# Kernel optimization log

Hardware: AMD Instinct MI355X
Metric: run time of the kernel (lower is better)

The kernel has to match this reference:

```python
import jax, jax.numpy as jnp
import numpy as np

BN_EPS = 1e-3      # Keras BatchNormalization default epsilon
LRELU_ALPHA = 0.3  # Keras LeakyReLU default alpha


def _bn(x, gamma, beta, mean, var):
    # inference-mode batch norm over the feature (last) axis
    return gamma * (x - mean) * jax.lax.rsqrt(var + BN_EPS) + beta


def _gcn(x, adj, w, b):
    # spektral GCNConv: A_hat @ (X @ W) + b   (adj assumed pre-normalized)
    xw = jnp.einsum('bnf,fc->bnc', x, w)
    return jnp.einsum('bnm,bmc->bnc', adj, xw) + b


def _lrelu(x):
    return jnp.where(x >= 0, x, LRELU_ALPHA * x)


def setup_inputs() -> dict:
    key = jax.random.key(0)
    ks = jax.random.split(key, 12)
    B, N, C = 16, 1024, 256
    x = jax.random.normal(ks[0], (B, N, C), dtype=jnp.float32)
    # roughly row-normalized dense adjacency (stands in for D^-1/2 (A+I) D^-1/2)
    adj = jax.random.uniform(ks[1], (B, N, N), dtype=jnp.float32) / N
    s = 1.0 / np.sqrt(C)
    return {
        'x': x,
        'adj': adj,
        'bn1_gamma': jnp.ones((C,), jnp.float32),
        'bn1_beta': jnp.zeros((C,), jnp.float32),
        'bn1_mean': jax.random.normal(ks[2], (C,), jnp.float32) * 0.1,
        'bn1_var': jax.random.uniform(ks[3], (C,), jnp.float32) + 0.5,
        'w1': jax.random.normal(ks[4], (C, C), jnp.float32) * s,
        'b1': jnp.zeros((C,), jnp.float32),
        'bn2_gamma': jnp.ones((C,), jnp.float32),
        'bn2_beta': jnp.zeros((C,), jnp.float32),
        'bn2_mean': jax.random.normal(ks[5], (C,), jnp.float32) * 0.1,
        'bn2_var': jax.random.uniform(ks[6], (C,), jnp.float32) + 0.5,
        'w2': jax.random.normal(ks[7], (C, C), jnp.float32) * s,
        'b2': jnp.zeros((C,), jnp.float32),
        'w_skip': jax.random.normal(ks[8], (C, C), jnp.float32) * s,
        'b_skip': jnp.zeros((C,), jnp.float32),
    }


def reference(x, adj, bn1_gamma, bn1_beta, bn1_mean, bn1_var, w1, b1,
              bn2_gamma, bn2_beta, bn2_mean, bn2_var, w2, b2, w_skip, b_skip):
    h = _bn(x, bn1_gamma, bn1_beta, bn1_mean, bn1_var)          # BN(input)
    out = _lrelu(_gcn(h, adj, w1, b1))                          # GCNConv + LeakyReLU
    out = _bn(out, bn2_gamma, bn2_beta, bn2_mean, bn2_var)      # BN
    out = _lrelu(_gcn(out, adj, w2, b2))                        # GCNConv + LeakyReLU
    skip = _gcn(h, adj, w_skip, b_skip)                         # skip GCNConv on BN(input)
    # Dropout is identity at inference
    return out + skip
```

## Files before the change

### kernel.cpp

```cpp
#include <hip/hip_runtime.h>

#define LRELU_ALPHA 0.3f
#define BN_EPS 1e-3f

using u16 = unsigned short;
using u32 = unsigned int;

typedef __attribute__((ext_vector_type(8))) short bf16x8;
typedef __attribute__((ext_vector_type(4))) float f32x4;

struct alignas(8) U16x4 { u16 x, y, z, w; };

__device__ __forceinline__ u16 f2bf(float f) {
  union { float f; u32 u; } v; v.f = f;
  u32 b = v.u;
  b += 0x7FFFu + ((b >> 16) & 1u);
  return (u16)(b >> 16);
}
__device__ __forceinline__ float bf2f(u16 h) {
  union { u32 u; float f; } v; v.u = ((u32)h) << 16;
  return v.f;
}

typedef const __attribute__((address_space(1))) void* gas_ptr;
typedef __attribute__((address_space(3))) void* las_ptr;

__device__ __forceinline__ void gload16(const void* g, void* l) {
  __builtin_amdgcn_global_load_lds((gas_ptr)g, (las_ptr)l, 16, 0, 0);
}

__device__ __forceinline__ int xcd_swz512(int lid) {
  return (lid & 7) * 64 + (lid >> 3);
}

template <int K>
__device__ __forceinline__ void gemm_core(const u16* __restrict__ A,
                                          const u16* __restrict__ B,
                                          u16* lds, f32x4 (&acc)[4][4]) {
  const int t = threadIdx.x, lane = t & 63, wid = t >> 6;
  const int wm = (wid >> 1) * 64, wn = (wid & 1) * 64;
  const int lrow = lane & 15, lk = (lane >> 4) * 8;
  const int r0 = t >> 3, ce = (t & 7) * 8, lo = wid * 512;
  u16* ldsA = lds;
  u16* ldsB = lds + 8192;
#pragma unroll 1
  for (int kt = 0; kt < K / 64; ++kt) {
    const u16* gA = A + kt * 64;
    const u16* gB = B + kt * 64;
#pragma unroll
    for (int cc = 0; cc < 4; ++cc) {
      gload16(gA + (size_t)(cc * 32 + r0) * K + ce, ldsA + cc * 2048 + lo);
      gload16(gB + (size_t)(cc * 32 + r0) * K + ce, ldsB + cc * 2048 + lo);
    }
    asm volatile("s_waitcnt vmcnt(0)" ::: "memory");
    __syncthreads();
#pragma unroll
    for (int kk = 0; kk < 2; ++kk) {
      bf16x8 a[4], b[4];
#pragma unroll
      for (int i = 0; i < 4; ++i)
        a[i] = *(const bf16x8*)(ldsA + (wm + i * 16 + lrow) * 64 + kk * 32 + lk);
#pragma unroll
      for (int i = 0; i < 4; ++i)
        b[i] = *(const bf16x8*)(ldsB + (wn + i * 16 + lrow) * 64 + kk * 32 + lk);
#pragma unroll
      for (int i = 0; i < 4; ++i)
#pragma unroll
        for (int j = 0; j < 4; ++j)
          acc[i][j] = __builtin_amdgcn_mfma_f32_16x16x32_bf16(a[i], b[j], acc[i][j], 0, 0, 0);
    }
    __syncthreads();
  }
}

template <int K>
__device__ __forceinline__ void gemm_core64(const u16* __restrict__ A,
                                            const u16* __restrict__ B,
                                            u16* lds, f32x4 (&acc)[2][4]) {
  const int t = threadIdx.x, lane = t & 63, wid = t >> 6;
  const int wm = wid * 32;
  const int lrow = lane & 15, lk = (lane >> 4) * 8;
  const int r0 = t >> 3, ce = (t & 7) * 8, lo = wid * 512;
  u16* ldsA = lds;
  u16* ldsB = lds + 8192;
#pragma unroll 1
  for (int kt = 0; kt < K / 64; ++kt) {
    const u16* gA = A + kt * 64;
    const u16* gB = B + kt * 64;
#pragma unroll
    for (int cc = 0; cc < 4; ++cc)
      gload16(gA + (size_t)(cc * 32 + r0) * K + ce, ldsA + cc * 2048 + lo);
#pragma unroll
    for (int cc = 0; cc < 2; ++cc)
      gload16(gB + (size_t)(cc * 32 + r0) * K + ce, ldsB + cc * 2048 + lo);
    asm volatile("s_waitcnt vmcnt(0)" ::: "memory");
    __syncthreads();
#pragma unroll
    for (int kk = 0; kk < 2; ++kk) {
      bf16x8 a[2], b[4];
#pragma unroll
      for (int i = 0; i < 2; ++i)
        a[i] = *(const bf16x8*)(ldsA + (wm + i * 16 + lrow) * 64 + kk * 32 + lk);
#pragma unroll
      for (int j = 0; j < 4; ++j)
        b[j] = *(const bf16x8*)(ldsB + (j * 16 + lrow) * 64 + kk * 32 + lk);
#pragma unroll
      for (int i = 0; i < 2; ++i)
#pragma unroll
        for (int j = 0; j < 4; ++j)
          acc[i][j] = __builtin_amdgcn_mfma_f32_16x16x32_bf16(a[i], b[j], acc[i][j], 0, 0, 0);
    }
    __syncthreads();
  }
}

template <int K>
__device__ __forceinline__ void gemm_core64x2(const u16* __restrict__ A,
                                              const u16* __restrict__ B1,
                                              const u16* __restrict__ B2,
                                              u16* lds, f32x4 (&acc1)[2][4],
                                              f32x4 (&acc2)[2][4]) {
  const int t = threadIdx.x, lane = t & 63, wid = t >> 6;
  const int wm = wid * 32;
  const int lrow = lane & 15, lk = (lane >> 4) * 8;
  const int r0 = t >> 3, ce = (t & 7) * 8, lo = wid * 512;
  u16* ldsA  = lds;
  u16* ldsB1 = lds + 8192;
  u16* ldsB2 = lds + 12288;
#pragma unroll 1
  for (int kt = 0; kt < K / 64; ++kt) {
    const u16* gA  = A  + kt * 64;
    const u16* gB1 = B1 + kt * 64;
    const u16* gB2 = B2 + kt * 64;
#pragma unroll
    for (int cc = 0; cc < 4; ++cc)
      gload16(gA + (size_t)(cc * 32 + r0) * K + ce, ldsA + cc * 2048 + lo);
#pragma unroll
    for (int cc = 0; cc < 2; ++cc) {
      gload16(gB1 + (size_t)(cc * 32 + r0) * K + ce, ldsB1 + cc * 2048 + lo);
      gload16(gB2 + (size_t)(cc * 32 + r0) * K + ce, ldsB2 + cc * 2048 + lo);
    }
    asm volatile("s_waitcnt vmcnt(0)" ::: "memory");
    __syncthreads();
#pragma unroll
    for (int kk = 0; kk < 2; ++kk) {
      bf16x8 a[2], b1[4], b2[4];
#pragma unroll
      for (int i = 0; i < 2; ++i)
        a[i] = *(const bf16x8*)(ldsA + (wm + i * 16 + lrow) * 64 + kk * 32 + lk);
#pragma unroll
      for (int j = 0; j < 4; ++j) {
        b1[j] = *(const bf16x8*)(ldsB1 + (j * 16 + lrow) * 64 + kk * 32 + lk);
        b2[j] = *(const bf16x8*)(ldsB2 + (j * 16 + lrow) * 64 + kk * 32 + lk);
      }
#pragma unroll
      for (int i = 0; i < 2; ++i)
#pragma unroll
        for (int j = 0; j < 4; ++j) {
          acc1[i][j] = __builtin_amdgcn_mfma_f32_16x16x32_bf16(a[i], b1[j], acc1[i][j], 0, 0, 0);
          acc2[i][j] = __builtin_amdgcn_mfma_f32_16x16x32_bf16(a[i], b2[j], acc2[i][j], 0, 0, 0);
        }
    }
    __syncthreads();
  }
}

#define ACC_INIT_N(name, R)                          \
  f32x4 name[R][4];                                  \
  _Pragma("unroll") for (int i_ = 0; i_ < R; ++i_)   \
  _Pragma("unroll") for (int j_ = 0; j_ < 4; ++j_)   \
      name[i_][j_] = {0.f, 0.f, 0.f, 0.f};

__global__ __launch_bounds__(256) void k_pre(
    const float* __restrict__ w1, const float* __restrict__ wsk, const float* __restrict__ w2,
    const float* __restrict__ g1, const float* __restrict__ be1,
    const float* __restrict__ m1, const float* __restrict__ v1,
    const float* __restrict__ g2, const float* __restrict__ be2,
    const float* __restrict__ m2, const float* __restrict__ v2,
    const float* __restrict__ x, const float* __restrict__ adj,
    u16* __restrict__ wcatT, u16* __restrict__ w2T,
    float* __restrict__ s2, float* __restrict__ t2c,
    u16* __restrict__ h_bf, u16* __restrict__ adj_bf) {
  int bid = blockIdx.x;
  if (bid < 768) {
    if (bid == 0) {
      int c = threadIdx.x;
      float a2 = g2[c] * rsqrtf(v2[c] + BN_EPS);
      s2[c] = a2;
      t2c[c] = be2[c] - m2[c] * a2;
    }
    int i = bid * 256 + threadIdx.x;
    if (i < 131072) {
      int co = i >> 8, ci = i & 255;
      const float* w = (co < 256) ? w1 : wsk;
      wcatT[i] = f2bf(w[ci * 256 + (co & 255)]);
    } else {
      int k = i - 131072;
      int co = k >> 8, ci = k & 255;
      w2T[k] = f2bf(w2[ci * 256 + co]);
    }
  } else if (bid < 1024) {
    int base = (bid - 768) * 256 + threadIdx.x;
    int c0 = (base << 2) & 255;
    float sc[4], sh[4];
#pragma unroll
    for (int u = 0; u < 4; ++u) {
      int c = c0 + u;
      float a = g1[c] * rsqrtf(v1[c] + BN_EPS);
      sc[u] = a;
      sh[u] = be1[c] - m1[c] * a;
    }
#pragma unroll
    for (int j = 0; j < 16; ++j) {
      int k = j * 65536 + base;
      float4 v = ((const float4*)x)[k];
      U16x4 o = {f2bf(v.x * sc[0] + sh[0]), f2bf(v.y * sc[1] + sh[1]),
                 f2bf(v.z * sc[2] + sh[2]), f2bf(v.w * sc[3] + sh[3])};
      ((U16x4*)h_bf)[k] = o;
    }
  } else {
    const int N4 = 4194304;
    int idx = (bid - 1024) * 256 + threadIdx.x;
    const int stride = 2048 * 256;
#pragma unroll 1
    for (; idx < N4; idx += stride) {
      float4 v = ((const float4*)adj)[idx];
      U16x4 o = {f2bf(v.x), f2bf(v.y), f2bf(v.z), f2bf(v.w)};
      ((U16x4*)adj_bf)[idx] = o;
    }
  }
}

__global__ __launch_bounds__(256) void k_xw(const u16* __restrict__ h_bf,
                                            const u16* __restrict__ wcatT,
                                            u16* __restrict__ hwT) {
  __shared__ u16 lds[17408];
  const int wg = xcd_swz512(blockIdx.x);
  const int mt = wg >> 2, nt = wg & 3;
  ACC_INIT_N(acc, 4);
  gemm_core<256>(h_bf + (size_t)mt * 128 * 256, wcatT + (size_t)nt * 128 * 256, lds, acc);

  const int t = threadIdx.x, lane = t & 63, wid = t >> 6;
  const int row0 = (wid >> 1) * 64 + (lane >> 4) * 4;
  const int col0 = (wid & 1) * 64 + (lane & 15);
  __syncthreads();
  u16* tl = lds;
#pragma unroll
  for (int j = 0; j < 4; ++j) {
    int co_l = col0 + j * 16;
#pragma unroll
    for (int i = 0; i < 4; ++i)
#pragma unroll
      for (int q = 0; q < 4; ++q)
        tl[co_l * 136 + row0 + i * 16 + q] = f2bf(acc[i][j][q]);
  }
  __syncthreads();
  const int rw = t >> 4, seg = t & 15;
  const int b = mt >> 3, nb = (mt & 7) * 128;
#pragma unroll
  for (int p = 0; p < 8; ++p) {
    int co_l = p * 16 + rw;
    *(bf16x8*)(hwT + (((size_t)(b * 512 + nt * 128 + co_l)) << 10) + nb + seg * 8) =
        *(const bf16x8*)(tl + co_l * 136 + seg * 8);
  }
}

__global__ __launch_bounds__(256) void k_big1(const u16* __restrict__ adj_bf,
                                              const u16* __restrict__ hwT,
                                              const float* __restrict__ b1,
                                              const float* __restrict__ s2,
                                              const float* __restrict__ t2c,
                                              u16* __restrict__ u2b) {
  __shared__ u16 lds[17408];
  ACC_INIT_N(acc, 2);
  const int wg = xcd_swz512(blockIdx.x);
  const int mt = wg & 7, nt = (wg >> 3) & 3, bz = wg >> 5;
  gemm_core64<1024>(adj_bf + ((size_t)bz << 20) + (size_t)mt * 128 * 1024,
                    hwT    + ((size_t)bz << 19) + ((size_t)(nt * 64) << 10), lds, acc);

  const int t = threadIdx.x, lane = t & 63, wid = t >> 6;
  const int row0 = wid * 32 + (lane >> 4) * 4;
  const int col0 = lane & 15;
  __syncthreads();
  u16* tl = lds;
#pragma unroll
  for (int j = 0; j < 4; ++j) {
    int cl = col0 + j * 16;
    int c = nt * 64 + cl;
    float bias = b1[c], sc = s2[c], tc = t2c[c];
#pragma unroll
    for (int i = 0; i < 2; ++i)
#pragma unroll
      for (int q = 0; q < 4; ++q) {
        float y = acc[i][j][q] + bias;
        float u = (y >= 0.f) ? y : LRELU_ALPHA * y;
        tl[(row0 + i * 16 + q) * 72 + cl] = f2bf(fmaf(u, sc, tc));
      }
  }
  __syncthreads();
  u16* dstbase = u2b + ((size_t)bz << 18) + nt * 64;
  const int rw = t >> 3, seg = t & 7;
#pragma unroll
  for (int p = 0; p < 4; ++p) {
    int nl = p * 32 + rw;
    *(bf16x8*)(dstbase + ((size_t)(mt * 128 + nl) << 8) + seg * 8) =
        *(const bf16x8*)(tl + nl * 72 + seg * 8);
  }
}

__global__ __launch_bounds__(256) void k_sm2(const u16* __restrict__ w2T,
                                             const u16* __restrict__ u2b,
                                             u16* __restrict__ t2T) {
  __shared__ u16 lds[12288];
  ACC_INIT_N(acc, 2);
  const int mt = blockIdx.x, nt = blockIdx.y, bz = blockIdx.z;
  gemm_core64<256>(w2T + (size_t)mt * 128 * 256,
                   u2b + ((size_t)bz << 18) + (size_t)nt * 64 * 256, lds, acc);

  const int t = threadIdx.x, lane = t & 63, wid = t >> 6;
  const int row0 = wid * 32 + (lane >> 4) * 4;
  const int col0 = lane & 15;
  __syncthreads();
  u16* tl = lds;
#pragma unroll
  for (int j = 0; j < 4; ++j)
#pragma unroll
    for (int i = 0; i < 2; ++i)
#pragma unroll
      for (int q = 0; q < 4; ++q)
        tl[(row0 + i * 16 + q) * 72 + col0 + j * 16] = f2bf(acc[i][j][q]);
  __syncthreads();
  u16* base = t2T + ((size_t)bz << 18) + nt * 64;
  const int rw = t >> 3, seg = t & 7;
#pragma unroll
  for (int p = 0; p < 4; ++p) {
    int co = p * 32 + rw;
    *(bf16x8*)(base + (((size_t)(mt * 128 + co)) << 10) + seg * 8) =
        *(const bf16x8*)(tl + co * 72 + seg * 8);
  }
}

__global__ __launch_bounds__(256) void k_big2(const u16* __restrict__ adj_bf,
                                              const u16* __restrict__ t2T,
                                              const u16* __restrict__ hwT,
                                              const float* __restrict__ b2,
                                              const float* __restrict__ bsk,
                                              float* __restrict__ outp) {
  __shared__ u16 lds[17408];
  ACC_INIT_N(acc1, 2);
  ACC_INIT_N(acc2, 2);
  const int wg = xcd_swz512(blockIdx.x);
  const int mt = wg & 7, nt = (wg >> 3) & 3, bz = wg >> 5;
  gemm_core64x2<1024>(adj_bf + ((size_t)bz << 20) + (size_t)mt * 128 * 1024,
                      t2T    + ((size_t)bz << 18) + ((size_t)(nt * 64) << 10),
                      hwT    + ((size_t)bz << 19) + ((size_t)(256 + nt * 64) << 10),
                      lds, acc1, acc2);

  const int t = threadIdx.x, lane = t & 63, wid = t >> 6;
  const int row0 = wid * 32 + (lane >> 4) * 4;
  const int col0 = lane & 15;
  __syncthreads();
  float* tf = (float*)lds;
#pragma unroll
  for (int j = 0; j < 4; ++j) {
    int cl = col0 + j * 16;
    int c = nt * 64 + cl;
    float bc = b2[c], bs = bsk[c];
#pragma unroll
    for (int i = 0; i < 2; ++i)
#pragma unroll
      for (int q = 0; q < 4; ++q) {
        float y = acc1[i][j][q] + bc;
        float conv = (y >= 0.f) ? y : LRELU_ALPHA * y;
        tf[(row0 + i * 16 + q) * 68 + cl] = conv + acc2[i][j][q] + bs;
      }
  }
  __syncthreads();
  const int rw = t >> 4, seg = t & 15;
#pragma unroll
  for (int p = 0; p < 8; ++p) {
    int nl = p * 16 + rw;
    size_t go = ((size_t)bz << 18) + ((size_t)(mt * 128 + nl) << 8) + nt * 64 + seg * 4;
    *(float4*)(outp + go) = *(const float4*)(tf + nl * 68 + seg * 4);
  }
}

extern "C" void kernel_launch(void* const* d_in, const int* in_sizes, int n_in,
                              void* d_out, int out_size, void* d_ws, size_t ws_size,
                              hipStream_t stream) {
  const float* x   = (const float*)d_in[0];
  const float* adj = (const float*)d_in[1];
  const float* g1  = (const float*)d_in[2];
  const float* be1 = (const float*)d_in[3];
  const float* mu1 = (const float*)d_in[4];
  const float* v1  = (const float*)d_in[5];
  const float* w1  = (const float*)d_in[6];
  const float* b1  = (const float*)d_in[7];
  const float* g2  = (const float*)d_in[8];
  const float* be2 = (const float*)d_in[9];
  const float* mu2 = (const float*)d_in[10];
  const float* v2  = (const float*)d_in[11];
  const float* w2  = (const float*)d_in[12];
  const float* b2  = (const float*)d_in[13];
  const float* wsk = (const float*)d_in[14];
  const float* bsk = (const float*)d_in[15];
  float* out = (float*)d_out;

  char* ws = (char*)d_ws;
  u16*   adj_bf = (u16*)(ws);
  u16*   hwT    = (u16*)(ws + 33554432);
  u16*   h_bf   = (u16*)(ws + 50331648);
  u16*   u2b    = (u16*)(ws + 58720256);
  u16*   t2T    = (u16*)(ws + 67108864);
  u16*   wcatT  = (u16*)(ws + 83886080);
  u16*   w2T    = (u16*)(ws + 84148224);
  float* s2     = (float*)(ws + 84281344);
  float* t2c    = (float*)(ws + 84282368);
  if (ws_size < 84283392) return;

  k_pre  <<<3072, 256, 0, stream>>>(w1, wsk, w2, g1, be1, mu1, v1, g2, be2, mu2, v2,
                                    x, adj, wcatT, w2T, s2, t2c, h_bf, adj_bf);
  k_xw   <<<512,  256, 0, stream>>>(h_bf, wcatT, hwT);
  k_big1 <<<512,  256, 0, stream>>>(adj_bf, hwT, b1, s2, t2c, u2b);
  k_sm2  <<<dim3(2, 16, 16), 256, 0, stream>>>(w2T, u2b, t2T);
  k_big2 <<<512,  256, 0, stream>>>(adj_bf, t2T, hwT, b2, bsk, out);
}
```

Before: 205.4 us.

## Fuse all stages into one persistent kernel with global atomic barriers

Merges the five kernels (convert/BN prep, X@W, first adjacency GEMM, W2 GEMM, second adjacency GEMM) into a single persistent 512-block kernel separated by software grid barriers built on atomics in workspace. The X@W stage is re-tiled to 64-wide output tiles, with each block doing two tiles. The goal is to remove kernel launch gaps and tail effects between stages. In exchange it adds a memset, global spin barriers and threadfences, and relies on all 512 blocks being co-resident; the prep stage also runs with fewer blocks than before.

```diff
diff --git a/kernel.cpp b/kernel.cpp
--- a/kernel.cpp
+++ b/kernel.cpp
@@ -17,10 +17,6 @@
   b += 0x7FFFu + ((b >> 16) & 1u);
   return (u16)(b >> 16);
 }
-__device__ __forceinline__ float bf2f(u16 h) {
-  union { u32 u; float f; } v; v.u = ((u32)h) << 16;
-  return v.f;
-}
 
 typedef const __attribute__((address_space(1))) void* gas_ptr;
 typedef __attribute__((address_space(3))) void* las_ptr;
@@ -33,44 +29,15 @@
   return (lid & 7) * 64 + (lid >> 3);
 }
 
-template <int K>
-__device__ __forceinline__ void gemm_core(const u16* __restrict__ A,
-                                          const u16* __restrict__ B,
-                                          u16* lds, f32x4 (&acc)[4][4]) {
-  const int t = threadIdx.x, lane = t & 63, wid = t >> 6;
-  const int wm = (wid >> 1) * 64, wn = (wid & 1) * 64;
-  const int lrow = lane & 15, lk = (lane >> 4) * 8;
-  const int r0 = t >> 3, ce = (t & 7) * 8, lo = wid * 512;
-  u16* ldsA = lds;
-  u16* ldsB = lds + 8192;
-#pragma unroll 1
-  for (int kt = 0; kt < K / 64; ++kt) {
-    const u16* gA = A + kt * 64;
-    const u16* gB = B + kt * 64;
-#pragma unroll
-    for (int cc = 0; cc < 4; ++cc) {
-      gload16(gA + (size_t)(cc * 32 + r0) * K + ce, ldsA + cc * 2048 + lo);
-      gload16(gB + (size_t)(cc * 32 + r0) * K + ce, ldsB + cc * 2048 + lo);
-    }
-    asm volatile("s_waitcnt vmcnt(0)" ::: "memory");
-    __syncthreads();
-#pragma unroll
-    for (int kk = 0; kk < 2; ++kk) {
-      bf16x8 a[4], b[4];
-#pragma unroll
-      for (int i = 0; i < 4; ++i)
-        a[i] = *(const bf16x8*)(ldsA + (wm + i * 16 + lrow) * 64 + kk * 32 + lk);
-#pragma unroll
-      for (int i = 0; i < 4; ++i)
-        b[i] = *(const bf16x8*)(ldsB + (wn + i * 16 + lrow) * 64 + kk * 32 + lk);
-#pragma unroll
-      for (int i = 0; i < 4; ++i)
-#pragma unroll
-        for (int j = 0; j < 4; ++j)
-          acc[i][j] = __builtin_amdgcn_mfma_f32_16x16x32_bf16(a[i], b[j], acc[i][j], 0, 0, 0);
-    }
-    __syncthreads();
-  }
+__device__ __forceinline__ void gbar(u32* bar, u32 nwg) {
+  __threadfence();
+  __syncthreads();
+  if (threadIdx.x == 0) {
+    atomicAdd(bar, 1u);
+    while (atomicAdd(bar, 0u) < nwg) __builtin_amdgcn_s_sleep(2);
+  }
+  __syncthreads();
+  __threadfence();
 }
 
 template <int K>
@@ -171,217 +138,205 @@
   _Pragma("unroll") for (int j_ = 0; j_ < 4; ++j_)   \
       name[i_][j_] = {0.f, 0.f, 0.f, 0.f};
 
-__global__ __launch_bounds__(256) void k_pre(
+__global__ __launch_bounds__(256, 2) void k_fused(
     const float* __restrict__ w1, const float* __restrict__ wsk, const float* __restrict__ w2,
     const float* __restrict__ g1, const float* __restrict__ be1,
     const float* __restrict__ m1, const float* __restrict__ v1,
     const float* __restrict__ g2, const float* __restrict__ be2,
     const float* __restrict__ m2, const float* __restrict__ v2,
     const float* __restrict__ x, const float* __restrict__ adj,
+    const float* __restrict__ b1, const float* __restrict__ b2,
+    const float* __restrict__ bsk,
     u16* __restrict__ wcatT, u16* __restrict__ w2T,
     float* __restrict__ s2, float* __restrict__ t2c,
-    u16* __restrict__ h_bf, u16* __restrict__ adj_bf) {
-  int bid = blockIdx.x;
-  if (bid < 768) {
-    if (bid == 0) {
-      int c = threadIdx.x;
+    u16* __restrict__ h_bf, u16* __restrict__ adj_bf,
+    u16* __restrict__ hwT, u16* __restrict__ u2b, u16* __restrict__ t2T,
+    u32* __restrict__ bars,
+    float* __restrict__ outp) {
+  __shared__ u16 lds[17408];
+  const int bidx = blockIdx.x;
+  const int t = threadIdx.x;
+  const int lane = t & 63, wid = t >> 6;
+
+  {
+    const int N4 = 4194304;
+#pragma unroll 1
+    for (int idx = bidx * 256 + t; idx < N4; idx += 131072) {
+      float4 v = ((const float4*)adj)[idx];
+      U16x4 o = {f2bf(v.x), f2bf(v.y), f2bf(v.z), f2bf(v.w)};
+      ((U16x4*)adj_bf)[idx] = o;
+    }
+    {
+      int idx0 = bidx * 256 + t;
+      int c0 = (idx0 << 2) & 255;
+      float sc[4], sh[4];
+#pragma unroll
+      for (int u = 0; u < 4; ++u) {
+        int c = c0 + u;
+        float a = g1[c] * rsqrtf(v1[c] + BN_EPS);
+        sc[u] = a;
+        sh[u] = be1[c] - m1[c] * a;
+      }
+#pragma unroll 1
+      for (int idx = idx0; idx < 1048576; idx += 131072) {
+        float4 v = ((const float4*)x)[idx];
+        U16x4 o = {f2bf(v.x * sc[0] + sh[0]), f2bf(v.y * sc[1] + sh[1]),
+                   f2bf(v.z * sc[2] + sh[2]), f2bf(v.w * sc[3] + sh[3])};
+        ((U16x4*)h_bf)[idx] = o;
+      }
+    }
+#pragma unroll 1
+    for (int i = bidx * 256 + t; i < 196608; i += 131072) {
+      if (i < 131072) {
+        int co = i >> 8, ci = i & 255;
+        const float* w = (co < 256) ? w1 : wsk;
+        wcatT[i] = f2bf(w[ci * 256 + (co & 255)]);
+      } else {
+        int k = i - 131072;
+        int co = k >> 8, ci = k & 255;
+        w2T[k] = f2bf(w2[ci * 256 + co]);
+      }
+    }
+    if (bidx == 0) {
+      int c = t;
       float a2 = g2[c] * rsqrtf(v2[c] + BN_EPS);
       s2[c] = a2;
       t2c[c] = be2[c] - m2[c] * a2;
     }
-    int i = bid * 256 + threadIdx.x;
-    if (i < 131072) {
-      int co = i >> 8, ci = i & 255;
-      const float* w = (co < 256) ? w1 : wsk;
-      wcatT[i] = f2bf(w[ci * 256 + (co & 255)]);
-    } else {
-      int k = i - 131072;
-      int co = k >> 8, ci = k & 255;
-      w2T[k] = f2bf(w2[ci * 256 + co]);
-    }
-  } else if (bid < 1024) {
-    int base = (bid - 768) * 256 + threadIdx.x;
-    int c0 = (base << 2) & 255;
-    float sc[4], sh[4];
-#pragma unroll
-    for (int u = 0; u < 4; ++u) {
-      int c = c0 + u;
-      float a = g1[c] * rsqrtf(v1[c] + BN_EPS);
-      sc[u] = a;
-      sh[u] = be1[c] - m1[c] * a;
-    }
-#pragma unroll
-    for (int j = 0; j < 16; ++j) {
-      int k = j * 65536 + base;
-      float4 v = ((const float4*)x)[k];
-      U16x4 o = {f2bf(v.x * sc[0] + sh[0]), f2bf(v.y * sc[1] + sh[1]),
-                 f2bf(v.z * sc[2] + sh[2]), f2bf(v.w * sc[3] + sh[3])};
-      ((U16x4*)h_bf)[k] = o;
-    }
-  } else {
-    const int N4 = 4194304;
-    int idx = (bid - 1024) * 256 + threadIdx.x;
-    const int stride = 2048 * 256;
-#pragma unroll 1
-    for (; idx < N4; idx += stride) {
-      float4 v = ((const float4*)adj)[idx];
-      U16x4 o = {f2bf(v.x), f2bf(v.y), f2bf(v.z), f2bf(v.w)};
-      ((U16x4*)adj_bf)[idx] = o;
-    }
-  }
-}
-
-__global__ __launch_bounds__(256) void k_xw(const u16* __restrict__ h_bf,
-                                            const u16* __restrict__ wcatT,
-                                            u16* __restrict__ hwT) {
-  __shared__ u16 lds[17408];
-  const int wg = xcd_swz512(blockIdx.x);
-  const int mt = wg >> 2, nt = wg & 3;
-  ACC_INIT_N(acc, 4);
-  gemm_core<256>(h_bf + (size_t)mt * 128 * 256, wcatT + (size_t)nt * 128 * 256, lds, acc);
-
-  const int t = threadIdx.x, lane = t & 63, wid = t >> 6;
-  const int row0 = (wid >> 1) * 64 + (lane >> 4) * 4;
-  const int col0 = (wid & 1) * 64 + (lane & 15);
-  __syncthreads();
-  u16* tl = lds;
-#pragma unroll
-  for (int j = 0; j < 4; ++j) {
-    int co_l = col0 + j * 16;
-#pragma unroll
-    for (int i = 0; i < 4; ++i)
-#pragma unroll
-      for (int q = 0; q < 4; ++q)
-        tl[co_l * 136 + row0 + i * 16 + q] = f2bf(acc[i][j][q]);
-  }
-  __syncthreads();
-  const int rw = t >> 4, seg = t & 15;
-  const int b = mt >> 3, nb = (mt & 7) * 128;
-#pragma unroll
-  for (int p = 0; p < 8; ++p) {
-    int co_l = p * 16 + rw;
-    *(bf16x8*)(hwT + (((size_t)(b * 512 + nt * 128 + co_l)) << 10) + nb + seg * 8) =
-        *(const bf16x8*)(tl + co_l * 136 + seg * 8);
-  }
-}
-
-__global__ __launch_bounds__(256) void k_big1(const u16* __restrict__ adj_bf,
-                                              const u16* __restrict__ hwT,
-                                              const float* __restrict__ b1,
-                                              const float* __restrict__ s2,
-                                              const float* __restrict__ t2c,
-                                              u16* __restrict__ u2b) {
-  __shared__ u16 lds[17408];
-  ACC_INIT_N(acc, 2);
-  const int wg = xcd_swz512(blockIdx.x);
-  const int mt = wg & 7, nt = (wg >> 3) & 3, bz = wg >> 5;
-  gemm_core64<1024>(adj_bf + ((size_t)bz << 20) + (size_t)mt * 128 * 1024,
-                    hwT    + ((size_t)bz << 19) + ((size_t)(nt * 64) << 10), lds, acc);
-
-  const int t = threadIdx.x, lane = t & 63, wid = t >> 6;
-  const int row0 = wid * 32 + (lane >> 4) * 4;
-  const int col0 = lane & 15;
-  __syncthreads();
-  u16* tl = lds;
-#pragma unroll
-  for (int j = 0; j < 4; ++j) {
-    int cl = col0 + j * 16;
-    int c = nt * 64 + cl;
-    float bias = b1[c], sc = s2[c], tc = t2c[c];
-#pragma unroll
-    for (int i = 0; i < 2; ++i)
-#pragma unroll
-      for (int q = 0; q < 4; ++q) {
-        float y = acc[i][j][q] + bias;
-        float u = (y >= 0.f) ? y : LRELU_ALPHA * y;
-        tl[(row0 + i * 16 + q) * 72 + cl] = f2bf(fmaf(u, sc, tc));
-      }
-  }
-  __syncthreads();
-  u16* dstbase = u2b + ((size_t)bz << 18) + nt * 64;
-  const int rw = t >> 3, seg = t & 7;
-#pragma unroll
-  for (int p = 0; p < 4; ++p) {
-    int nl = p * 32 + rw;
-    *(bf16x8*)(dstbase + ((size_t)(mt * 128 + nl) << 8) + seg * 8) =
-        *(const bf16x8*)(tl + nl * 72 + seg * 8);
-  }
-}
-
-__global__ __launch_bounds__(256) void k_sm2(const u16* __restrict__ w2T,
-                                             const u16* __restrict__ u2b,
-                                             u16* __restrict__ t2T) {
-  __shared__ u16 lds[12288];
-  ACC_INIT_N(acc, 2);
-  const int mt = blockIdx.x, nt = blockIdx.y, bz = blockIdx.z;
-  gemm_core64<256>(w2T + (size_t)mt * 128 * 256,
-                   u2b + ((size_t)bz << 18) + (size_t)nt * 64 * 256, lds, acc);
-
-  const int t = threadIdx.x, lane = t & 63, wid = t >> 6;
-  const int row0 = wid * 32 + (lane >> 4) * 4;
-  const int col0 = lane & 15;
-  __syncthreads();
-  u16* tl = lds;
-#pragma unroll
-  for (int j = 0; j < 4; ++j)
-#pragma unroll
-    for (int i = 0; i < 2; ++i)
-#pragma unroll
-      for (int q = 0; q < 4; ++q)
-        tl[(row0 + i * 16 + q) * 72 + col0 + j * 16] = f2bf(acc[i][j][q]);
-  __syncthreads();
-  u16* base = t2T + ((size_t)bz << 18) + nt * 64;
-  const int rw = t >> 3, seg = t & 7;
-#pragma unroll
-  for (int p = 0; p < 4; ++p) {
-    int co = p * 32 + rw;
-    *(bf16x8*)(base + (((size_t)(mt * 128 + co)) << 10) + seg * 8) =
-        *(const bf16x8*)(tl + co * 72 + seg * 8);
-  }
-}
-
-__global__ __launch_bounds__(256) void k_big2(const u16* __restrict__ adj_bf,
-                                              const u16* __restrict__ t2T,
-                                              const u16* __restrict__ hwT,
-                                              const float* __restrict__ b2,
-                                              const float* __restrict__ bsk,
-                                              float* __restrict__ outp) {
-  __shared__ u16 lds[17408];
-  ACC_INIT_N(acc1, 2);
-  ACC_INIT_N(acc2, 2);
-  const int wg = xcd_swz512(blockIdx.x);
-  const int mt = wg & 7, nt = (wg >> 3) & 3, bz = wg >> 5;
-  gemm_core64x2<1024>(adj_bf + ((size_t)bz << 20) + (size_t)mt * 128 * 1024,
-                      t2T    + ((size_t)bz << 18) + ((size_t)(nt * 64) << 10),
-                      hwT    + ((size_t)bz << 19) + ((size_t)(256 + nt * 64) << 10),
-                      lds, acc1, acc2);
-
-  const int t = threadIdx.x, lane = t & 63, wid = t >> 6;
-  const int row0 = wid * 32 + (lane >> 4) * 4;
-  const int col0 = lane & 15;
-  __syncthreads();
-  float* tf = (float*)lds;
-#pragma unroll
-  for (int j = 0; j < 4; ++j) {
-    int cl = col0 + j * 16;
-    int c = nt * 64 + cl;
-    float bc = b2[c], bs = bsk[c];
-#pragma unroll
-    for (int i = 0; i < 2; ++i)
-#pragma unroll
-      for (int q = 0; q < 4; ++q) {
-        float y = acc1[i][j][q] + bc;
-        float conv = (y >= 0.f) ? y : LRELU_ALPHA * y;
-        tf[(row0 + i * 16 + q) * 68 + cl] = conv + acc2[i][j][q] + bs;
-      }
-  }
-  __syncthreads();
-  const int rw = t >> 4, seg = t & 15;
-#pragma unroll
-  for (int p = 0; p < 8; ++p) {
-    int nl = p * 16 + rw;
-    size_t go = ((size_t)bz << 18) + ((size_t)(mt * 128 + nl) << 8) + nt * 64 + seg * 4;
-    *(float4*)(outp + go) = *(const float4*)(tf + nl * 68 + seg * 4);
+  }
+  gbar(bars + 0, 512);
+
+  {
+    const int wg = xcd_swz512(bidx);
+#pragma unroll 1
+    for (int half = 0; half < 2; ++half) {
+      const int tau = wg + half * 512;
+      const int mt = tau >> 3, nt = tau & 7;
+      ACC_INIT_N(acc, 2);
+      gemm_core64<256>(h_bf + (size_t)mt * 128 * 256,
+                       wcatT + (size_t)nt * 64 * 256, lds, acc);
+      const int row0 = wid * 32 + (lane >> 4) * 4;
+      const int col0 = lane & 15;
+      u16* tl = lds;
+#pragma unroll
+      for (int j = 0; j < 4; ++j) {
+        int cl = col0 + j * 16;
+#pragma unroll
+        for (int i = 0; i < 2; ++i)
+#pragma unroll
+          for (int q = 0; q < 4; ++q)
+            tl[cl * 136 + row0 + i * 16 + q] = f2bf(acc[i][j][q]);
+      }
+      __syncthreads();
+      const int rw = t >> 4, seg = t & 15;
+      const int bb = mt >> 3, nb = (mt & 7) * 128;
+#pragma unroll
+      for (int p = 0; p < 4; ++p) {
+        int cl = p * 16 + rw;
+        *(bf16x8*)(hwT + (((size_t)(bb * 512 + nt * 64 + cl)) << 10) + nb + seg * 8) =
+            *(const bf16x8*)(tl + cl * 136 + seg * 8);
+      }
+      __syncthreads();
+    }
+  }
+  gbar(bars + 1, 512);
+
+  {
+    const int wg = xcd_swz512(bidx);
+    const int mt = wg & 7, nt = (wg >> 3) & 3, bz = wg >> 5;
+    ACC_INIT_N(acc, 2);
+    gemm_core64<1024>(adj_bf + ((size_t)bz << 20) + (size_t)mt * 128 * 1024,
+                      hwT    + ((size_t)bz << 19) + ((size_t)(nt * 64) << 10), lds, acc);
+    const int row0 = wid * 32 + (lane >> 4) * 4;
+    const int col0 = lane & 15;
+    u16* tl = lds;
+#pragma unroll
+    for (int j = 0; j < 4; ++j) {
+      int cl = col0 + j * 16;
+      int c = nt * 64 + cl;
+      float bias = b1[c], sc = s2[c], tc = t2c[c];
+#pragma unroll
+      for (int i = 0; i < 2; ++i)
+#pragma unroll
+        for (int q = 0; q < 4; ++q) {
+          float y = acc[i][j][q] + bias;
+          float u = (y >= 0.f) ? y : LRELU_ALPHA * y;
+          tl[(row0 + i * 16 + q) * 72 + cl] = f2bf(fmaf(u, sc, tc));
+        }
+    }
+    __syncthreads();
+    u16* dstbase = u2b + ((size_t)bz << 18) + nt * 64;
+    const int rw = t >> 3, seg = t & 7;
+#pragma unroll
+    for (int p = 0; p < 4; ++p) {
+      int nl = p * 32 + rw;
+      *(bf16x8*)(dstbase + ((size_t)(mt * 128 + nl) << 8) + seg * 8) =
+          *(const bf16x8*)(tl + nl * 72 + seg * 8);
+    }
+  }
+  gbar(bars + 2, 512);
+
+  {
+    const int mt = bidx & 1, nt = (bidx >> 1) & 15, bz = bidx >> 5;
+    ACC_INIT_N(acc, 2);
+    gemm_core64<256>(w2T + (size_t)mt * 128 * 256,
+                     u2b + ((size_t)bz << 18) + (size_t)nt * 64 * 256, lds, acc);
+    const int row0 = wid * 32 + (lane >> 4) * 4;
+    const int col0 = lane & 15;
+    u16* tl = lds;
+#pragma unroll
+    for (int j = 0; j < 4; ++j)
+#pragma unroll
+      for (int i = 0; i < 2; ++i)
+#pragma unroll
+        for (int q = 0; q < 4; ++q)
+          tl[(row0 + i * 16 + q) * 72 + col0 + j * 16] = f2bf(acc[i][j][q]);
+    __syncthreads();
+    u16* base = t2T + ((size_t)bz << 18) + nt * 64;
+    const int rw = t >> 3, seg = t & 7;
+#pragma unroll
+    for (int p = 0; p < 4; ++p) {
+      int co = p * 32 + rw;
+      *(bf16x8*)(base + (((size_t)(mt * 128 + co)) << 10) + seg * 8) =
+          *(const bf16x8*)(tl + co * 72 + seg * 8);
+    }
+  }
+  gbar(bars + 3, 512);
+
+  {
+    const int wg = xcd_swz512(bidx);
+    const int mt = wg & 7, nt = (wg >> 3) & 3, bz = wg >> 5;
+    ACC_INIT_N(acc1, 2);
+    ACC_INIT_N(acc2, 2);
+    gemm_core64x2<1024>(adj_bf + ((size_t)bz << 20) + (size_t)mt * 128 * 1024,
+                        t2T    + ((size_t)bz << 18) + ((size_t)(nt * 64) << 10),
+                        hwT    + ((size_t)bz << 19) + ((size_t)(256 + nt * 64) << 10),
+                        lds, acc1, acc2);
+    const int row0 = wid * 32 + (lane >> 4) * 4;
+    const int col0 = lane & 15;
+    float* tf = (float*)lds;
+#pragma unroll
+    for (int j = 0; j < 4; ++j) {
+      int cl = col0 + j * 16;
+      int c = nt * 64 + cl;
+      float bc = b2[c], bs = bsk[c];
+#pragma unroll
+      for (int i = 0; i < 2; ++i)
+#pragma unroll
+        for (int q = 0; q < 4; ++q) {
+          float y = acc1[i][j][q] + bc;
+          float conv = (y >= 0.f) ? y : LRELU_ALPHA * y;
+          tf[(row0 + i * 16 + q) * 68 + cl] = conv + acc2[i][j][q] + bs;
+        }
+    }
+    __syncthreads();
+    const int rw = t >> 4, seg = t & 15;
+#pragma unroll
+    for (int p = 0; p < 8; ++p) {
+      int nl = p * 16 + rw;
+      size_t go = ((size_t)bz << 18) + ((size_t)(mt * 128 + nl) << 8) + nt * 64 + seg * 4;
+      *(float4*)(outp + go) = *(const float4*)(tf + nl * 68 + seg * 4);
+    }
   }
 }
 
@@ -412,16 +367,15 @@
   u16*   h_bf   = (u16*)(ws + 50331648);
   u16*   u2b    = (u16*)(ws + 58720256);
   u16*   t2T    = (u16*)(ws + 67108864);
+  u32*   bars   = (u32*)(ws + 75497472);
   u16*   wcatT  = (u16*)(ws + 83886080);
   u16*   w2T    = (u16*)(ws + 84148224);
   float* s2     = (float*)(ws + 84281344);
   float* t2c    = (float*)(ws + 84282368);
   if (ws_size < 84283392) return;
 
-  k_pre  <<<3072, 256, 0, stream>>>(w1, wsk, w2, g1, be1, mu1, v1, g2, be2, mu2, v2,
-                                    x, adj, wcatT, w2T, s2, t2c, h_bf, adj_bf);
-  k_xw   <<<512,  256, 0, stream>>>(h_bf, wcatT, hwT);
-  k_big1 <<<512,  256, 0, stream>>>(adj_bf, hwT, b1, s2, t2c, u2b);
-  k_sm2  <<<dim3(2, 16, 16), 256, 0, stream>>>(w2T, u2b, t2T);
-  k_big2 <<<512,  256, 0, stream>>>(adj_bf, t2T, hwT, b2, bsk, out);
-}
+  hipMemsetAsync((void*)bars, 0, 64, stream);
+  k_fused<<<512, 256, 0, stream>>>(
+      w1, wsk, w2, g1, be1, mu1, v1, g2, be2, mu2, v2, x, adj,
+      b1, b2, bsk, wcatT, w2T, s2, t2c, h_bf, adj_bf, hwT, u2b, t2T, bars, out);
+}
```

Result: slower. 632.3 us (+207.9%).
